# Performance work log

Measured on AMD Instinct MI355X. Metric: run time of the kernel, lower is better.

## Reference

```python
import jax, jax.numpy as jnp
import numpy as np

# Model dims: D=input_dim, H=hidden_dim, E=num_experts, k=1
B, T, D, H, E = 4, 1024, 1024, 4096, 8
ALPHA = BETA = GAMMA = 0.001


def setup_inputs() -> dict:
    key = jax.random.key(0)
    ks = jax.random.split(key, 6)
    s = 0.02
    return {
        "x": jax.random.normal(ks[0], (B, T, D), jnp.float32),
        "gate_w": jax.random.normal(ks[1], (D, E), jnp.float32) * s,
        "gate_b": jnp.zeros((E,), jnp.float32),
        "w1": jax.random.normal(ks[2], (E, D, H), jnp.float32) * s,
        "b1": jnp.zeros((E, H), jnp.float32),
        "w2": jax.random.normal(ks[3], (E, H, D), jnp.float32) * s,
        "b2": jnp.zeros((E, D), jnp.float32),
    }


def reference(x, gate_w, gate_b, w1, b1, w2, b2):
    Bs, Ts, Ds = x.shape
    N = Bs * Ts
    nE = gate_w.shape[1]
    xf = x.reshape(N, Ds)

    logits = xf @ gate_w + gate_b                      # (N, E)
    probs = jax.nn.softmax(logits, axis=-1)            # (N, E)
    # k=1 top-k == argmax
    top1 = jnp.argmax(logits, axis=-1)                 # (N,) int
    top1_p = jnp.take_along_axis(probs, top1[:, None], axis=-1)[:, 0]  # (N,)
    m = jax.nn.one_hot(top1, nE, dtype=x.dtype)        # (N, E) routing mask
    counts = m.sum(axis=0)                             # (E,) tokens per expert
    safe = jnp.maximum(counts, 1.0)

    # Dense per-expert FFN on all tokens (baseline for sparse dispatch)
    h = jax.nn.relu(jnp.einsum('nd,edh->enh', xf, w1) + b1[:, None, :])   # (E,N,H)
    y = jnp.einsum('enh,ehd->end', h, w2) + b2[:, None, :]                # (E,N,D)

    # Per-expert scalar avg prob of selected tokens (module multiplies by the MEAN prob)
    avg_p = jnp.where(counts > 0, (m * top1_p[:, None]).sum(axis=0) / safe, 0.0)  # (E,)
    out = jnp.einsum('ne,e,end->nd', m, avg_p, y)      # masked combine

    # Load-balancing aux loss
    usage = counts / N
    aux_loss = (usage ** 2).sum() * nE

    # Orthogonality loss: for each expert, G = Y_e Y_e^T over its tokens,
    # mean of squared off-diagonals. Computed via ||Y^T Y||_F^2 trick (DxD)
    ym = y * jnp.transpose(m)[:, :, None]              # (E,N,D) masked outputs
    M = jnp.einsum('end,enc->edc', ym, ym)             # (E,D,D) = Y^T Y per expert
    sq_norms = (ym ** 2).sum(axis=-1)                  # (E,N) diag of Gram
    off_sq_sum = (M ** 2).sum(axis=(1, 2)) - (sq_norms ** 2).sum(axis=1)  # (E,)
    orth_loss = jnp.where(counts > 0, off_sq_sum / (safe ** 2), 0.0).sum()

    # Variance loss
    var_loss = -((probs - probs.mean(axis=0)) ** 2).mean()

    total_loss = ALPHA * aux_loss + BETA * orth_loss + GAMMA * var_loss
    return out.reshape(Bs, Ts, Ds), total_loss
```

## Files before the change

kernel.cpp:

```cpp
#include <hip/hip_runtime.h>
#include <stdint.h>

#define TOKENS 4096
#define DIM    1024
#define HDIM   4096
#define NEXP   8
#define NPAD   5120
#define ALPHA  0.001f
#define BETA   0.001f
#define GAMMA  0.001f

#define WS_CNT      0
#define WS_SUMP     32
#define WS_PSUM     64
#define WS_PSUMSQ   96
#define WS_OFFP     128
#define WS_AVGP     192
#define WS_LOSSP    224
#define WS_OFFSQ    256
#define WS_HDR_END  512
#define WS_YNORM    512
#define WS_LIST     21504
#define WS_XB       152576
#define WS_W1T      8541184
#define WS_W2T      75650048
#define WS_HBUF     142758912
#define WS_YT       184701952
#define WS_TOTAL    195187712

typedef __bf16 bf16x8 __attribute__((ext_vector_type(8)));
typedef float  f32x4  __attribute__((ext_vector_type(4)));
typedef unsigned short u16x4 __attribute__((ext_vector_type(4)));

__device__ __forceinline__ unsigned short f2bf(float f) {
    union { float f; unsigned u; } v; v.f = f;
    unsigned r = v.u + 0x7fffu + ((v.u >> 16) & 1u);
    return (unsigned short)(r >> 16);
}
__device__ __forceinline__ float bf2f(unsigned short h) {
    union { unsigned u; float f; } v; v.u = ((unsigned)h) << 16;
    return v.f;
}

__global__ void k_cvt_x(const float* __restrict__ x, unsigned short* __restrict__ xb) {
    const int n4 = TOKENS * DIM / 4;
    for (int i = blockIdx.x * blockDim.x + threadIdx.x; i < n4; i += gridDim.x * blockDim.x) {
        float4 v = ((const float4*)x)[i];
        u16x4 o;
        o[0] = f2bf(v.x); o[1] = f2bf(v.y); o[2] = f2bf(v.z); o[3] = f2bf(v.w);
        ((u16x4*)xb)[i] = o;
    }
}

__global__ void k_transpose_cvt(const float* __restrict__ in, unsigned short* __restrict__ out,
                                int R, int C) {
    __shared__ float tile[32][33];
    const float* inp = in + (size_t)blockIdx.z * R * C;
    unsigned short* outp = out + (size_t)blockIdx.z * R * C;
    int r0 = blockIdx.y * 32, c0 = blockIdx.x * 32;
    int tx = threadIdx.x & 31, ty = threadIdx.x >> 5;
#pragma unroll
    for (int j = 0; j < 4; j++)
        tile[ty + 8 * j][tx] = inp[(size_t)(r0 + ty + 8 * j) * C + c0 + tx];
    __syncthreads();
#pragma unroll
    for (int j = 0; j < 4; j++)
        outp[(size_t)(c0 + ty + 8 * j) * R + r0 + tx] = f2bf(tile[tx][ty + 8 * j]);
}

__global__ __launch_bounds__(1024) void k_gate(
        const float* __restrict__ x, const float* __restrict__ gw, const float* __restrict__ gb,
        int* __restrict__ cnt, float* __restrict__ sump,
        float* __restrict__ psum, float* __restrict__ psumsq, int* __restrict__ list) {
    __shared__ float gwT[NEXP * DIM];
    __shared__ float bacc[3 * NEXP];
    int tid = threadIdx.x;
    if (tid < 3 * NEXP) bacc[tid] = 0.f;
    for (int i = tid; i < DIM * NEXP; i += 1024) {
        int d = i >> 3, e = i & 7;
        gwT[e * DIM + d] = gw[i];
    }
    __syncthreads();
    int wv = tid >> 6, l = tid & 63;
    int t = blockIdx.x * 16 + wv;
    float acc[8];
#pragma unroll
    for (int e = 0; e < 8; e++) acc[e] = 0.f;
    const float* xr = x + (size_t)t * DIM;
#pragma unroll
    for (int j = 0; j < 16; j++) {
        float xv = xr[l + 64 * j];
#pragma unroll
        for (int e = 0; e < 8; e++) acc[e] += xv * gwT[e * DIM + l + 64 * j];
    }
#pragma unroll
    for (int e = 0; e < 8; e++) {
#pragma unroll
        for (int s = 32; s > 0; s >>= 1) acc[e] += __shfl_xor(acc[e], s);
    }
    if (l == 0) {
        float lg[8], mx = -1e30f;
#pragma unroll
        for (int e = 0; e < 8; e++) { lg[e] = acc[e] + gb[e]; mx = fmaxf(mx, lg[e]); }
        float p[8], se = 0.f;
#pragma unroll
        for (int e = 0; e < 8; e++) { p[e] = __expf(lg[e] - mx); se += p[e]; }
        float inv = 1.f / se;
        int arg = 0; float best = lg[0];
#pragma unroll
        for (int e = 1; e < 8; e++) if (lg[e] > best) { best = lg[e]; arg = e; }
        float ptop = p[arg] * inv;
        int pos = atomicAdd(&cnt[arg], 1);
        list[arg * TOKENS + pos] = t;
        atomicAdd(&bacc[arg], ptop);
#pragma unroll
        for (int e = 0; e < 8; e++) {
            float pe = p[e] * inv;
            atomicAdd(&bacc[8 + e], pe);
            atomicAdd(&bacc[16 + e], pe * pe);
        }
    }
    __syncthreads();
    if (tid < 8) {
        atomicAdd(&sump[tid], bacc[tid]);
        atomicAdd(&psum[tid], bacc[8 + tid]);
        atomicAdd(&psumsq[tid], bacc[16 + tid]);
    }
}

__global__ void k_finalize_gate(const int* __restrict__ cnt, const float* __restrict__ sump,
                                const float* __restrict__ psum, const float* __restrict__ psumsq,
                                int* __restrict__ offp, float* __restrict__ avgp,
                                float* __restrict__ lossp) {
    if (threadIdx.x == 0) {
        int off = 0; float aux = 0.f, var = 0.f;
        for (int e = 0; e < 8; e++) {
            offp[e] = off;
            int c = cnt[e];
            off += ((c + 127) / 128) * 128;
            float cf = (float)c;
            avgp[e] = (c > 0) ? sump[e] / cf : 0.f;
            float u = cf / (float)TOKENS;
            aux += u * u;
            var += psumsq[e] - psum[e] * psum[e] / (float)TOKENS;
        }
        offp[8] = off;
        aux *= (float)NEXP;
        float varloss = -var / ((float)TOKENS * (float)NEXP);
        lossp[0] = ALPHA * aux + GAMMA * varloss;
    }
}

__global__ __launch_bounds__(256) void k_gemm1(
        const unsigned short* __restrict__ xb, const unsigned short* __restrict__ w1t,
        const float* __restrict__ b1, const int* __restrict__ cnt, const int* __restrict__ offp,
        const int* __restrict__ list, unsigned short* __restrict__ Hbuf) {
    int e = blockIdx.z, rt = blockIdx.y, ct = blockIdx.x;
    int cnt_e = cnt[e];
    int row0 = rt * 128;
    if (row0 >= cnt_e) return;
    int offe = offp[e];
    __shared__ unsigned short ldsA[128 * 32];
    __shared__ unsigned short ldsB[128 * 32];
    int tid = threadIdx.x, wv = tid >> 6, l = tid & 63;
    int wr = wv >> 1, wc = wv & 1;
    int r0s = l, r1s = 64 + l;
    int t0 = list[e * TOKENS + min(row0 + r0s, cnt_e - 1)];
    int t1 = list[e * TOKENS + min(row0 + r1s, cnt_e - 1)];
    const unsigned short* srcA0 = xb + (size_t)t0 * DIM + wv * 8;
    const unsigned short* srcA1 = xb + (size_t)t1 * DIM + wv * 8;
    const unsigned short* srcB0 = w1t + ((size_t)e * HDIM + ct * 128 + r0s) * DIM + wv * 8;
    const unsigned short* srcB1 = w1t + ((size_t)e * HDIM + ct * 128 + r1s) * DIM + wv * 8;
    f32x4 acc[4][4] = {};
    for (int kk = 0; kk < DIM; kk += 32) {
        bf16x8 va0 = *(const bf16x8*)(srcA0 + kk);
        bf16x8 va1 = *(const bf16x8*)(srcA1 + kk);
        bf16x8 vb0 = *(const bf16x8*)(srcB0 + kk);
        bf16x8 vb1 = *(const bf16x8*)(srcB1 + kk);
        __syncthreads();
        *(bf16x8*)(ldsA + (wv * 128 + l) * 8)      = va0;
        *(bf16x8*)(ldsA + (wv * 128 + 64 + l) * 8) = va1;
        *(bf16x8*)(ldsB + (wv * 128 + l) * 8)      = vb0;
        *(bf16x8*)(ldsB + (wv * 128 + 64 + l) * 8) = vb1;
        __syncthreads();
        int g = l >> 4, rr = l & 15;
        bf16x8 a[4], b[4];
#pragma unroll
        for (int m = 0; m < 4; m++) a[m] = *(const bf16x8*)(ldsA + (g * 128 + wr * 64 + m * 16 + rr) * 8);
#pragma unroll
        for (int n = 0; n < 4; n++) b[n] = *(const bf16x8*)(ldsB + (g * 128 + wc * 64 + n * 16 + rr) * 8);
#pragma unroll
        for (int m = 0; m < 4; m++)
#pragma unroll
            for (int n = 0; n < 4; n++)
                acc[m][n] = __builtin_amdgcn_mfma_f32_16x16x32_bf16(a[m], b[n], acc[m][n], 0, 0, 0);
    }
    int g = l >> 4, rr = l & 15;
#pragma unroll
    for (int n = 0; n < 4; n++) {
        int colg = ct * 128 + wc * 64 + n * 16 + rr;
        float bv = b1[e * HDIM + colg];
#pragma unroll
        for (int m = 0; m < 4; m++) {
#pragma unroll
            for (int j = 0; j < 4; j++) {
                int rloc = row0 + wr * 64 + m * 16 + g * 4 + j;
                if (rloc < cnt_e) {
                    float v = fmaxf(acc[m][n][j] + bv, 0.f);
                    Hbuf[(size_t)(offe + rloc) * HDIM + colg] = f2bf(v);
                }
            }
        }
    }
}

__global__ __launch_bounds__(256) void k_gemm2(
        const unsigned short* __restrict__ Hbuf, const unsigned short* __restrict__ w2t,
        const float* __restrict__ b2, const int* __restrict__ cnt, const int* __restrict__ offp,
        const int* __restrict__ list, const float* __restrict__ avgp,
        float* __restrict__ out, unsigned short* __restrict__ yT) {
    int e = blockIdx.z, rt = blockIdx.y, ct = blockIdx.x;
    int cnt_e = cnt[e];
    int row0 = rt * 128;
    if (row0 >= cnt_e) return;
    int offe = offp[e];
    __shared__ unsigned short ldsA[128 * 32];
    __shared__ unsigned short ldsB[128 * 32];
    int tid = threadIdx.x, wv = tid >> 6, l = tid & 63;
    int wr = wv >> 1, wc = wv & 1;
    int r0s = l, r1s = 64 + l;
    const unsigned short* srcA0 = Hbuf + (size_t)(offe + row0 + r0s) * HDIM + wv * 8;
    const unsigned short* srcA1 = Hbuf + (size_t)(offe + row0 + r1s) * HDIM + wv * 8;
    const unsigned short* srcB0 = w2t + ((size_t)e * DIM + ct * 128 + r0s) * HDIM + wv * 8;
    const unsigned short* srcB1 = w2t + ((size_t)e * DIM + ct * 128 + r1s) * HDIM + wv * 8;
    f32x4 acc[4][4] = {};
    for (int kk = 0; kk < HDIM; kk += 32) {
        bf16x8 va0 = *(const bf16x8*)(srcA0 + kk);
        bf16x8 va1 = *(const bf16x8*)(srcA1 + kk);
        bf16x8 vb0 = *(const bf16x8*)(srcB0 + kk);
        bf16x8 vb1 = *(const bf16x8*)(srcB1 + kk);
        __syncthreads();
        *(bf16x8*)(ldsA + (wv * 128 + l) * 8)      = va0;
        *(bf16x8*)(ldsA + (wv * 128 + 64 + l) * 8) = va1;
        *(bf16x8*)(ldsB + (wv * 128 + l) * 8)      = vb0;
        *(bf16x8*)(ldsB + (wv * 128 + 64 + l) * 8) = vb1;
        __syncthreads();
        int g = l >> 4, rr = l & 15;
        bf16x8 a[4], b[4];
#pragma unroll
        for (int m = 0; m < 4; m++) a[m] = *(const bf16x8*)(ldsA + (g * 128 + wr * 64 + m * 16 + rr) * 8);
#pragma unroll
        for (int n = 0; n < 4; n++) b[n] = *(const bf16x8*)(ldsB + (g * 128 + wc * 64 + n * 16 + rr) * 8);
#pragma unroll
        for (int m = 0; m < 4; m++)
#pragma unroll
            for (int n = 0; n < 4; n++)
                acc[m][n] = __builtin_amdgcn_mfma_f32_16x16x32_bf16(a[m], b[n], acc[m][n], 0, 0, 0);
    }
    float ap = avgp[e];
    int g = l >> 4, rr = l & 15;
#pragma unroll
    for (int m = 0; m < 4; m++) {
        int rbase = row0 + wr * 64 + m * 16 + g * 4;
        int toks[4]; bool lv[4];
#pragma unroll
        for (int j = 0; j < 4; j++) {
            int rl = rbase + j;
            lv[j] = rl < cnt_e;
            toks[j] = lv[j] ? list[e * TOKENS + rl] : 0;
        }
#pragma unroll
        for (int n = 0; n < 4; n++) {
            int colg = ct * 128 + wc * 64 + n * 16 + rr;
            float bv = b2[e * DIM + colg];
            u16x4 pk;
#pragma unroll
            for (int j = 0; j < 4; j++) {
                float yv = acc[m][n][j] + bv;
                if (lv[j]) {
                    out[(size_t)toks[j] * DIM + colg] = ap * yv;
                    pk[j] = f2bf(yv);
                } else {
                    pk[j] = 0;
                }
            }
            *(u16x4*)(yT + (size_t)colg * NPAD + offe + rbase) = pk;
        }
    }
}

__global__ void k_ynorm(const unsigned short* __restrict__ yT, float* __restrict__ ynorm) {
    int n = blockIdx.x * blockDim.x + threadIdx.x;
    if (n >= NPAD) return;
    float s = 0.f;
    for (int d = 0; d < DIM; d++) {
        float v = bf2f(yT[(size_t)d * NPAD + n]);
        s += v * v;
    }
    ynorm[n] = s;
}

__global__ __launch_bounds__(256) void k_gram(
        const unsigned short* __restrict__ yT, const int* __restrict__ cnt,
        const int* __restrict__ offp, float* __restrict__ offsq) {
    int e = blockIdx.z, dt = blockIdx.y, ct = blockIdx.x;
    int cnt_e = cnt[e];
    if (cnt_e <= 0) return;
    int offe = offp[e];
    int ksteps = (cnt_e + 31) / 32;
    __shared__ unsigned short ldsA[128 * 32];
    __shared__ unsigned short ldsB[128 * 32];
    __shared__ float wsum[4];
    int tid = threadIdx.x, wv = tid >> 6, l = tid & 63;
    int wr = wv >> 1, wc = wv & 1;
    int r0s = l, r1s = 64 + l;
    const unsigned short* srcA0 = yT + (size_t)(dt * 128 + r0s) * NPAD + offe + wv * 8;
    const unsigned short* srcA1 = yT + (size_t)(dt * 128 + r1s) * NPAD + offe + wv * 8;
    const unsigned short* srcB0 = yT + (size_t)(ct * 128 + r0s) * NPAD + offe + wv * 8;
    const unsigned short* srcB1 = yT + (size_t)(ct * 128 + r1s) * NPAD + offe + wv * 8;
    f32x4 acc[4][4] = {};
    for (int ks = 0; ks < ksteps; ks++) {
        int kk = ks * 32;
        bf16x8 va0 = *(const bf16x8*)(srcA0 + kk);
        bf16x8 va1 = *(const bf16x8*)(srcA1 + kk);
        bf16x8 vb0 = *(const bf16x8*)(srcB0 + kk);
        bf16x8 vb1 = *(const bf16x8*)(srcB1 + kk);
        __syncthreads();
        *(bf16x8*)(ldsA + (wv * 128 + l) * 8)      = va0;
        *(bf16x8*)(ldsA + (wv * 128 + 64 + l) * 8) = va1;
        *(bf16x8*)(ldsB + (wv * 128 + l) * 8)      = vb0;
        *(bf16x8*)(ldsB + (wv * 128 + 64 + l) * 8) = vb1;
        __syncthreads();
        int g = l >> 4, rr = l & 15;
        bf16x8 a[4], b[4];
#pragma unroll
        for (int m = 0; m < 4; m++) a[m] = *(const bf16x8*)(ldsA + (g * 128 + wr * 64 + m * 16 + rr) * 8);
#pragma unroll
        for (int n = 0; n < 4; n++) b[n] = *(const bf16x8*)(ldsB + (g * 128 + wc * 64 + n * 16 + rr) * 8);
#pragma unroll
        for (int m = 0; m < 4; m++)
#pragma unroll
            for (int n = 0; n < 4; n++)
                acc[m][n] = __builtin_amdgcn_mfma_f32_16x16x32_bf16(a[m], b[n], acc[m][n], 0, 0, 0);
    }
    float s = 0.f;
#pragma unroll
    for (int m = 0; m < 4; m++)
#pragma unroll
        for (int n = 0; n < 4; n++)
#pragma unroll
            for (int j = 0; j < 4; j++) s += acc[m][n][j] * acc[m][n][j];
#pragma unroll
    for (int sh = 32; sh > 0; sh >>= 1) s += __shfl_xor(s, sh);
    if (l == 0) wsum[wv] = s;
    __syncthreads();
    if (tid == 0) atomicAdd(&offsq[e], wsum[0] + wsum[1] + wsum[2] + wsum[3]);
}

__global__ void k_loss(const int* __restrict__ cnt, const int* __restrict__ offp,
                       const float* __restrict__ offsq, const float* __restrict__ ynorm,
                       const float* __restrict__ lossp, float* __restrict__ out_loss) {
    __shared__ float ssq[8];
    int tid = threadIdx.x;
    if (tid < 8) ssq[tid] = 0.f;
    __syncthreads();
    int total = offp[8];
    for (int i = tid; i < total; i += blockDim.x) {
        int e = 0;
#pragma unroll
        for (int k = 0; k < 8; k++) if (i >= offp[k + 1]) e = k + 1;
        float s = ynorm[i];
        atomicAdd(&ssq[e], s * s);
    }
    __syncthreads();
    if (tid == 0) {
        float orth = 0.f;
        for (int e = 0; e < 8; e++) {
            if (cnt[e] > 0) {
                float cf = (float)cnt[e];
                orth += (offsq[e] - ssq[e]) / (cf * cf);
            }
        }
        out_loss[0] = lossp[0] + BETA * orth;
    }
}

extern "C" void kernel_launch(void* const* d_in, const int* in_sizes, int n_in,
                              void* d_out, int out_size, void* d_ws, size_t ws_size,
                              hipStream_t stream) {
    (void)in_sizes; (void)n_in; (void)out_size;
    const float* x  = (const float*)d_in[0];
    const float* gw = (const float*)d_in[1];
    const float* gb = (const float*)d_in[2];
    const float* w1 = (const float*)d_in[3];
    const float* b1 = (const float*)d_in[4];
    const float* w2 = (const float*)d_in[5];
    const float* b2 = (const float*)d_in[6];
    float* out = (float*)d_out;
    char* ws = (char*)d_ws;
    if (ws_size < (size_t)WS_TOTAL) return;

    int*   cnt    = (int*)(ws + WS_CNT);
    float* sump   = (float*)(ws + WS_SUMP);
    float* psum   = (float*)(ws + WS_PSUM);
    float* psumsq = (float*)(ws + WS_PSUMSQ);
    int*   offp   = (int*)(ws + WS_OFFP);
    float* avgp   = (float*)(ws + WS_AVGP);
    float* lossp  = (float*)(ws + WS_LOSSP);
    float* offsq  = (float*)(ws + WS_OFFSQ);
    float* ynorm  = (float*)(ws + WS_YNORM);
    int*   list   = (int*)(ws + WS_LIST);
    unsigned short* xb   = (unsigned short*)(ws + WS_XB);
    unsigned short* w1t  = (unsigned short*)(ws + WS_W1T);
    unsigned short* w2t  = (unsigned short*)(ws + WS_W2T);
    unsigned short* Hbuf = (unsigned short*)(ws + WS_HBUF);
    unsigned short* yT   = (unsigned short*)(ws + WS_YT);

    hipMemsetAsync(ws, 0, WS_HDR_END, stream);
    k_cvt_x<<<2048, 256, 0, stream>>>(x, xb);
    k_transpose_cvt<<<dim3(128, 32, 8), 256, 0, stream>>>(w1, w1t, 1024, 4096);
    k_transpose_cvt<<<dim3(32, 128, 8), 256, 0, stream>>>(w2, w2t, 4096, 1024);
    k_gate<<<256, 1024, 0, stream>>>(x, gw, gb, cnt, sump, psum, psumsq, list);
    k_finalize_gate<<<1, 64, 0, stream>>>(cnt, sump, psum, psumsq, offp, avgp, lossp);
    k_gemm1<<<dim3(32, 32, 8), 256, 0, stream>>>(xb, w1t, b1, cnt, offp, list, Hbuf);
    k_gemm2<<<dim3(8, 32, 8), 256, 0, stream>>>(Hbuf, w2t, b2, cnt, offp, list, avgp, out, yT);
    k_ynorm<<<20, 256, 0, stream>>>(yT, ynorm);
    k_gram<<<dim3(8, 8, 8), 256, 0, stream>>>(yT, cnt, offp, offsq);
    k_loss<<<1, 256, 0, stream>>>(cnt, offp, offsq, ynorm, lossp, out + (size_t)TOKENS * DIM);
}
```

Baseline: 858.9 us.

## Compact grids, register double-buffer GEMMs, split-K gemm2, fuse combine and ynorm

The GEMM grids are compacted so each block derives its expert from the padded row offset instead of launching empty blocks per expert. All three MFMA kernels gain a two-stage register prefetch of global loads. gemm2 is split in two along K, writing fp32 partials into a buffer that reuses the w1t region. A new combine kernel sums the partials, adds the bias, scatters the scaled output and writes yT, and accumulates row norms with atomics, which replaces the separate ynorm kernel. The transpose now uses 64x64 tiles. The cost is extra fp32 partial-buffer traffic, atomics, and reuse of the w1t region, which is safe only because gemm1 has finished by then.

```diff
diff --git a/kernel.cpp b/kernel.cpp
--- a/kernel.cpp
+++ b/kernel.cpp
@@ -18,8 +18,8 @@
 #define WS_AVGP     192
 #define WS_LOSSP    224
 #define WS_OFFSQ    256
-#define WS_HDR_END  512
 #define WS_YNORM    512
+#define WS_ZERO_END 20992
 #define WS_LIST     21504
 #define WS_XB       152576
 #define WS_W1T      8541184
@@ -27,6 +27,8 @@
 #define WS_HBUF     142758912
 #define WS_YT       184701952
 #define WS_TOTAL    195187712
+#define WS_YBUF     WS_W1T
+#define YBS         (NPAD * DIM)
 
 typedef __bf16 bf16x8 __attribute__((ext_vector_type(8)));
 typedef float  f32x4  __attribute__((ext_vector_type(4)));
@@ -36,10 +38,6 @@
     union { float f; unsigned u; } v; v.f = f;
     unsigned r = v.u + 0x7fffu + ((v.u >> 16) & 1u);
     return (unsigned short)(r >> 16);
-}
-__device__ __forceinline__ float bf2f(unsigned short h) {
-    union { unsigned u; float f; } v; v.u = ((unsigned)h) << 16;
-    return v.f;
 }
 
 __global__ void k_cvt_x(const float* __restrict__ x, unsigned short* __restrict__ xb) {
@@ -52,20 +50,20 @@
     }
 }
 
-__global__ void k_transpose_cvt(const float* __restrict__ in, unsigned short* __restrict__ out,
-                                int R, int C) {
-    __shared__ float tile[32][33];
+__global__ __launch_bounds__(256) void k_transpose_cvt(
+        const float* __restrict__ in, unsigned short* __restrict__ out, int R, int C) {
+    __shared__ float tile[64][65];
     const float* inp = in + (size_t)blockIdx.z * R * C;
     unsigned short* outp = out + (size_t)blockIdx.z * R * C;
-    int r0 = blockIdx.y * 32, c0 = blockIdx.x * 32;
-    int tx = threadIdx.x & 31, ty = threadIdx.x >> 5;
-#pragma unroll
-    for (int j = 0; j < 4; j++)
-        tile[ty + 8 * j][tx] = inp[(size_t)(r0 + ty + 8 * j) * C + c0 + tx];
-    __syncthreads();
-#pragma unroll
-    for (int j = 0; j < 4; j++)
-        outp[(size_t)(c0 + ty + 8 * j) * R + r0 + tx] = f2bf(tile[tx][ty + 8 * j]);
+    int r0 = blockIdx.y * 64, c0 = blockIdx.x * 64;
+    int tx = threadIdx.x & 63, ty = threadIdx.x >> 6;
+#pragma unroll
+    for (int j = 0; j < 16; j++)
+        tile[ty + 4 * j][tx] = inp[(size_t)(r0 + ty + 4 * j) * C + c0 + tx];
+    __syncthreads();
+#pragma unroll
+    for (int j = 0; j < 16; j++)
+        outp[(size_t)(c0 + ty + 4 * j) * R + r0 + tx] = f2bf(tile[tx][ty + 4 * j]);
 }
 
 __global__ __launch_bounds__(1024) void k_gate(
@@ -155,34 +153,49 @@
         const unsigned short* __restrict__ xb, const unsigned short* __restrict__ w1t,
         const float* __restrict__ b1, const int* __restrict__ cnt, const int* __restrict__ offp,
         const int* __restrict__ list, unsigned short* __restrict__ Hbuf) {
-    int e = blockIdx.z, rt = blockIdx.y, ct = blockIdx.x;
-    int cnt_e = cnt[e];
-    int row0 = rt * 128;
-    if (row0 >= cnt_e) return;
-    int offe = offp[e];
     __shared__ unsigned short ldsA[128 * 32];
     __shared__ unsigned short ldsB[128 * 32];
+    int ct = blockIdx.x, rt = blockIdx.y;
+    int prow0 = rt * 128;
+    if (prow0 >= offp[8]) return;
+    int e = 0;
+#pragma unroll
+    for (int k = 1; k < 8; k++) if (prow0 >= offp[k]) e = k;
+    int offe = offp[e], row0 = prow0 - offe, cnt_e = cnt[e];
     int tid = threadIdx.x, wv = tid >> 6, l = tid & 63;
     int wr = wv >> 1, wc = wv & 1;
-    int r0s = l, r1s = 64 + l;
-    int t0 = list[e * TOKENS + min(row0 + r0s, cnt_e - 1)];
-    int t1 = list[e * TOKENS + min(row0 + r1s, cnt_e - 1)];
+    int t0 = list[e * TOKENS + min(row0 + l, cnt_e - 1)];
+    int t1 = list[e * TOKENS + min(row0 + 64 + l, cnt_e - 1)];
     const unsigned short* srcA0 = xb + (size_t)t0 * DIM + wv * 8;
     const unsigned short* srcA1 = xb + (size_t)t1 * DIM + wv * 8;
-    const unsigned short* srcB0 = w1t + ((size_t)e * HDIM + ct * 128 + r0s) * DIM + wv * 8;
-    const unsigned short* srcB1 = w1t + ((size_t)e * HDIM + ct * 128 + r1s) * DIM + wv * 8;
+    const unsigned short* srcB0 = w1t + ((size_t)e * HDIM + ct * 128 + l) * DIM + wv * 8;
+    const unsigned short* srcB1 = w1t + ((size_t)e * HDIM + ct * 128 + 64 + l) * DIM + wv * 8;
     f32x4 acc[4][4] = {};
-    for (int kk = 0; kk < DIM; kk += 32) {
-        bf16x8 va0 = *(const bf16x8*)(srcA0 + kk);
-        bf16x8 va1 = *(const bf16x8*)(srcA1 + kk);
-        bf16x8 vb0 = *(const bf16x8*)(srcB0 + kk);
-        bf16x8 vb1 = *(const bf16x8*)(srcB1 + kk);
-        __syncthreads();
-        *(bf16x8*)(ldsA + (wv * 128 + l) * 8)      = va0;
-        *(bf16x8*)(ldsA + (wv * 128 + 64 + l) * 8) = va1;
-        *(bf16x8*)(ldsB + (wv * 128 + l) * 8)      = vb0;
-        *(bf16x8*)(ldsB + (wv * 128 + 64 + l) * 8) = vb1;
-        __syncthreads();
+    bf16x8 sa0[2], sa1[2], sb0[2], sb1[2];
+    const int NK = DIM / 32;
+#pragma unroll
+    for (int p = 0; p < 2; p++) {
+        int kk = p * 32;
+        sa0[p] = *(const bf16x8*)(srcA0 + kk);
+        sa1[p] = *(const bf16x8*)(srcA1 + kk);
+        sb0[p] = *(const bf16x8*)(srcB0 + kk);
+        sb1[p] = *(const bf16x8*)(srcB1 + kk);
+    }
+    for (int i = 0; i < NK; i++) {
+        int cur = i & 1;
+        __syncthreads();
+        *(bf16x8*)(ldsA + (wv * 128 + l) * 8)      = sa0[cur];
+        *(bf16x8*)(ldsA + (wv * 128 + 64 + l) * 8) = sa1[cur];
+        *(bf16x8*)(ldsB + (wv * 128 + l) * 8)      = sb0[cur];
+        *(bf16x8*)(ldsB + (wv * 128 + 64 + l) * 8) = sb1[cur];
+        __syncthreads();
+        if (i + 2 < NK) {
+            int kk = (i + 2) * 32;
+            sa0[cur] = *(const bf16x8*)(srcA0 + kk);
+            sa1[cur] = *(const bf16x8*)(srcA1 + kk);
+            sb0[cur] = *(const bf16x8*)(srcB0 + kk);
+            sb1[cur] = *(const bf16x8*)(srcB1 + kk);
+        }
         int g = l >> 4, rr = l & 15;
         bf16x8 a[4], b[4];
 #pragma unroll
@@ -216,35 +229,50 @@
 
 __global__ __launch_bounds__(256) void k_gemm2(
         const unsigned short* __restrict__ Hbuf, const unsigned short* __restrict__ w2t,
-        const float* __restrict__ b2, const int* __restrict__ cnt, const int* __restrict__ offp,
-        const int* __restrict__ list, const float* __restrict__ avgp,
-        float* __restrict__ out, unsigned short* __restrict__ yT) {
-    int e = blockIdx.z, rt = blockIdx.y, ct = blockIdx.x;
-    int cnt_e = cnt[e];
-    int row0 = rt * 128;
-    if (row0 >= cnt_e) return;
-    int offe = offp[e];
+        const int* __restrict__ cnt, const int* __restrict__ offp,
+        float* __restrict__ ybuf) {
     __shared__ unsigned short ldsA[128 * 32];
     __shared__ unsigned short ldsB[128 * 32];
+    int ct = blockIdx.x, rt = blockIdx.y, s = blockIdx.z;
+    int prow0 = rt * 128;
+    if (prow0 >= offp[8]) return;
+    int e = 0;
+#pragma unroll
+    for (int k = 1; k < 8; k++) if (prow0 >= offp[k]) e = k;
+    int offe = offp[e];
     int tid = threadIdx.x, wv = tid >> 6, l = tid & 63;
     int wr = wv >> 1, wc = wv & 1;
-    int r0s = l, r1s = 64 + l;
-    const unsigned short* srcA0 = Hbuf + (size_t)(offe + row0 + r0s) * HDIM + wv * 8;
-    const unsigned short* srcA1 = Hbuf + (size_t)(offe + row0 + r1s) * HDIM + wv * 8;
-    const unsigned short* srcB0 = w2t + ((size_t)e * DIM + ct * 128 + r0s) * HDIM + wv * 8;
-    const unsigned short* srcB1 = w2t + ((size_t)e * DIM + ct * 128 + r1s) * HDIM + wv * 8;
+    const size_t kbase = (size_t)s * (HDIM / 2) + wv * 8;
+    const unsigned short* srcA0 = Hbuf + (size_t)(prow0 + l) * HDIM + kbase;
+    const unsigned short* srcA1 = Hbuf + (size_t)(prow0 + 64 + l) * HDIM + kbase;
+    const unsigned short* srcB0 = w2t + ((size_t)e * DIM + ct * 128 + l) * HDIM + kbase;
+    const unsigned short* srcB1 = w2t + ((size_t)e * DIM + ct * 128 + 64 + l) * HDIM + kbase;
     f32x4 acc[4][4] = {};
-    for (int kk = 0; kk < HDIM; kk += 32) {
-        bf16x8 va0 = *(const bf16x8*)(srcA0 + kk);
-        bf16x8 va1 = *(const bf16x8*)(srcA1 + kk);
-        bf16x8 vb0 = *(const bf16x8*)(srcB0 + kk);
-        bf16x8 vb1 = *(const bf16x8*)(srcB1 + kk);
-        __syncthreads();
-        *(bf16x8*)(ldsA + (wv * 128 + l) * 8)      = va0;
-        *(bf16x8*)(ldsA + (wv * 128 + 64 + l) * 8) = va1;
-        *(bf16x8*)(ldsB + (wv * 128 + l) * 8)      = vb0;
-        *(bf16x8*)(ldsB + (wv * 128 + 64 + l) * 8) = vb1;
-        __syncthreads();
+    bf16x8 sa0[2], sa1[2], sb0[2], sb1[2];
+    const int NK = HDIM / 2 / 32;
+#pragma unroll
+    for (int p = 0; p < 2; p++) {
+        int kk = p * 32;
+        sa0[p] = *(const bf16x8*)(srcA0 + kk);
+        sa1[p] = *(const bf16x8*)(srcA1 + kk);
+        sb0[p] = *(const bf16x8*)(srcB0 + kk);
+        sb1[p] = *(const bf16x8*)(srcB1 + kk);
+    }
+    for (int i = 0; i < NK; i++) {
+        int cur = i & 1;
+        __syncthreads();
+        *(bf16x8*)(ldsA + (wv * 128 + l) * 8)      = sa0[cur];
+        *(bf16x8*)(ldsA + (wv * 128 + 64 + l) * 8) = sa1[cur];
+        *(bf16x8*)(ldsB + (wv * 128 + l) * 8)      = sb0[cur];
+        *(bf16x8*)(ldsB + (wv * 128 + 64 + l) * 8) = sb1[cur];
+        __syncthreads();
+        if (i + 2 < NK) {
+            int kk = (i + 2) * 32;
+            sa0[cur] = *(const bf16x8*)(srcA0 + kk);
+            sa1[cur] = *(const bf16x8*)(srcA1 + kk);
+            sb0[cur] = *(const bf16x8*)(srcB0 + kk);
+            sb1[cur] = *(const bf16x8*)(srcB1 + kk);
+        }
         int g = l >> 4, rr = l & 15;
         bf16x8 a[4], b[4];
 #pragma unroll
@@ -257,80 +285,105 @@
             for (int n = 0; n < 4; n++)
                 acc[m][n] = __builtin_amdgcn_mfma_f32_16x16x32_bf16(a[m], b[n], acc[m][n], 0, 0, 0);
     }
-    float ap = avgp[e];
+    float* yb = ybuf + (size_t)s * YBS;
     int g = l >> 4, rr = l & 15;
 #pragma unroll
-    for (int m = 0; m < 4; m++) {
-        int rbase = row0 + wr * 64 + m * 16 + g * 4;
-        int toks[4]; bool lv[4];
-#pragma unroll
-        for (int j = 0; j < 4; j++) {
-            int rl = rbase + j;
-            lv[j] = rl < cnt_e;
-            toks[j] = lv[j] ? list[e * TOKENS + rl] : 0;
-        }
+    for (int m = 0; m < 4; m++)
 #pragma unroll
         for (int n = 0; n < 4; n++) {
             int colg = ct * 128 + wc * 64 + n * 16 + rr;
-            float bv = b2[e * DIM + colg];
-            u16x4 pk;
 #pragma unroll
             for (int j = 0; j < 4; j++) {
-                float yv = acc[m][n][j] + bv;
-                if (lv[j]) {
-                    out[(size_t)toks[j] * DIM + colg] = ap * yv;
-                    pk[j] = f2bf(yv);
-                } else {
-                    pk[j] = 0;
-                }
+                int prow = prow0 + wr * 64 + m * 16 + g * 4 + j;
+                yb[(size_t)prow * DIM + colg] = acc[m][n][j];
             }
-            *(u16x4*)(yT + (size_t)colg * NPAD + offe + rbase) = pk;
-        }
-    }
-}
-
-__global__ void k_ynorm(const unsigned short* __restrict__ yT, float* __restrict__ ynorm) {
-    int n = blockIdx.x * blockDim.x + threadIdx.x;
-    if (n >= NPAD) return;
-    float s = 0.f;
-    for (int d = 0; d < DIM; d++) {
-        float v = bf2f(yT[(size_t)d * NPAD + n]);
-        s += v * v;
-    }
-    ynorm[n] = s;
+        }
+}
+
+__global__ __launch_bounds__(256) void k_combine(
+        const float* __restrict__ ybuf, const float* __restrict__ b2,
+        const int* __restrict__ cnt, const int* __restrict__ offp,
+        const int* __restrict__ list, const float* __restrict__ avgp,
+        float* __restrict__ out, unsigned short* __restrict__ yT,
+        float* __restrict__ ynorm) {
+    int dt = blockIdx.x, rt = blockIdx.y;
+    int prow0 = rt * 128;
+    if (prow0 >= offp[8]) return;
+    int e = 0;
+#pragma unroll
+    for (int k = 1; k < 8; k++) if (prow0 >= offp[k]) e = k;
+    int offe = offp[e], cnt_e = cnt[e];
+    float ap = avgp[e];
+    int tid = threadIdx.x, l = tid & 63, w = tid >> 6;
+    int d = dt * 64 + l;
+    float bv = b2[e * DIM + d];
+    for (int q = w * 8; q < w * 8 + 8; q++) {
+        int prow = prow0 + q * 4;
+        u16x4 pk;
+        float ys2[4];
+#pragma unroll
+        for (int j = 0; j < 4; j++) {
+            int pr = prow + j;
+            int rl = pr - offe;
+            float yv = ybuf[(size_t)pr * DIM + d] + ybuf[(size_t)YBS + (size_t)pr * DIM + d] + bv;
+            bool valid = rl < cnt_e;
+            if (valid) out[(size_t)list[e * TOKENS + rl] * DIM + d] = ap * yv;
+            pk[j] = valid ? f2bf(yv) : (unsigned short)0;
+            ys2[j] = valid ? yv * yv : 0.f;
+        }
+        *(u16x4*)(yT + (size_t)d * NPAD + prow) = pk;
+#pragma unroll
+        for (int j = 0; j < 4; j++) {
+            float sv = ys2[j];
+#pragma unroll
+            for (int sh = 32; sh > 0; sh >>= 1) sv += __shfl_xor(sv, sh);
+            if (l == 0) atomicAdd(&ynorm[prow + j], sv);
+        }
+    }
 }
 
 __global__ __launch_bounds__(256) void k_gram(
         const unsigned short* __restrict__ yT, const int* __restrict__ cnt,
         const int* __restrict__ offp, float* __restrict__ offsq) {
+    __shared__ unsigned short ldsA[128 * 32];
+    __shared__ unsigned short ldsB[128 * 32];
+    __shared__ float wsum[4];
     int e = blockIdx.z, dt = blockIdx.y, ct = blockIdx.x;
     int cnt_e = cnt[e];
     if (cnt_e <= 0) return;
     int offe = offp[e];
-    int ksteps = (cnt_e + 31) / 32;
-    __shared__ unsigned short ldsA[128 * 32];
-    __shared__ unsigned short ldsB[128 * 32];
-    __shared__ float wsum[4];
+    int NK = (offp[e + 1] - offe) >> 5;
     int tid = threadIdx.x, wv = tid >> 6, l = tid & 63;
     int wr = wv >> 1, wc = wv & 1;
-    int r0s = l, r1s = 64 + l;
-    const unsigned short* srcA0 = yT + (size_t)(dt * 128 + r0s) * NPAD + offe + wv * 8;
-    const unsigned short* srcA1 = yT + (size_t)(dt * 128 + r1s) * NPAD + offe + wv * 8;
-    const unsigned short* srcB0 = yT + (size_t)(ct * 128 + r0s) * NPAD + offe + wv * 8;
-    const unsigned short* srcB1 = yT + (size_t)(ct * 128 + r1s) * NPAD + offe + wv * 8;
+    const unsigned short* srcA0 = yT + (size_t)(dt * 128 + l) * NPAD + offe + wv * 8;
+    const unsigned short* srcA1 = yT + (size_t)(dt * 128 + 64 + l) * NPAD + offe + wv * 8;
+    const unsigned short* srcB0 = yT + (size_t)(ct * 128 + l) * NPAD + offe + wv * 8;
+    const unsigned short* srcB1 = yT + (size_t)(ct * 128 + 64 + l) * NPAD + offe + wv * 8;
     f32x4 acc[4][4] = {};
-    for (int ks = 0; ks < ksteps; ks++) {
-        int kk = ks * 32;
-        bf16x8 va0 = *(const bf16x8*)(srcA0 + kk);
-        bf16x8 va1 = *(const bf16x8*)(srcA1 + kk);
-        bf16x8 vb0 = *(const bf16x8*)(srcB0 + kk);
-        bf16x8 vb1 = *(const bf16x8*)(srcB1 + kk);
-        __syncthreads();
-        *(bf16x8*)(ldsA + (wv * 128 + l) * 8)      = va0;
-        *(bf16x8*)(ldsA + (wv * 128 + 64 + l) * 8) = va1;
-        *(bf16x8*)(ldsB + (wv * 128 + l) * 8)      = vb0;
-        *(bf16x8*)(ldsB + (wv * 128 + 64 + l) * 8) = vb1;
-        __syncthreads();
+    bf16x8 sa0[2], sa1[2], sb0[2], sb1[2];
+#pragma unroll
+    for (int p = 0; p < 2; p++) {
+        int kk = p * 32;
+        sa0[p] = *(const bf16x8*)(srcA0 + kk);
+        sa1[p] = *(const bf16x8*)(srcA1 + kk);
+        sb0[p] = *(const bf16x8*)(srcB0 + kk);
+        sb1[p] = *(const bf16x8*)(srcB1 + kk);
+    }
+    for (int i = 0; i < NK; i++) {
+        int cur = i & 1;
+        __syncthreads();
+        *(bf16x8*)(ldsA + (wv * 128 + l) * 8)      = sa0[cur];
+        *(bf16x8*)(ldsA + (wv * 128 + 64 + l) * 8) = sa1[cur];
+        *(bf16x8*)(ldsB + (wv * 128 + l) * 8)      = sb0[cur];
+        *(bf16x8*)(ldsB + (wv * 128 + 64 + l) * 8) = sb1[cur];
+        __syncthreads();
+        if (i + 2 < NK) {
+            int kk = (i + 2) * 32;
+            sa0[cur] = *(const bf16x8*)(srcA0 + kk);
+            sa1[cur] = *(const bf16x8*)(srcA1 + kk);
+            sb0[cur] = *(const bf16x8*)(srcB0 + kk);
+            sb1[cur] = *(const bf16x8*)(srcB1 + kk);
+        }
         int g = l >> 4, rr = l & 15;
         bf16x8 a[4], b[4];
 #pragma unroll
@@ -415,16 +468,17 @@
     unsigned short* w2t  = (unsigned short*)(ws + WS_W2T);
     unsigned short* Hbuf = (unsigned short*)(ws + WS_HBUF);
     unsigned short* yT   = (unsigned short*)(ws + WS_YT);
-
-    hipMemsetAsync(ws, 0, WS_HDR_END, stream);
+    float* ybuf          = (float*)(ws + WS_YBUF);
+
+    hipMemsetAsync(ws, 0, WS_ZERO_END, stream);
     k_cvt_x<<<2048, 256, 0, stream>>>(x, xb);
-    k_transpose_cvt<<<dim3(128, 32, 8), 256, 0, stream>>>(w1, w1t, 1024, 4096);
-    k_transpose_cvt<<<dim3(32, 128, 8), 256, 0, stream>>>(w2, w2t, 4096, 1024);
+    k_transpose_cvt<<<dim3(64, 16, 8), 256, 0, stream>>>(w1, w1t, 1024, 4096);
+    k_transpose_cvt<<<dim3(16, 64, 8), 256, 0, stream>>>(w2, w2t, 4096, 1024);
     k_gate<<<256, 1024, 0, stream>>>(x, gw, gb, cnt, sump, psum, psumsq, list);
     k_finalize_gate<<<1, 64, 0, stream>>>(cnt, sump, psum, psumsq, offp, avgp, lossp);
-    k_gemm1<<<dim3(32, 32, 8), 256, 0, stream>>>(xb, w1t, b1, cnt, offp, list, Hbuf);
-    k_gemm2<<<dim3(8, 32, 8), 256, 0, stream>>>(Hbuf, w2t, b2, cnt, offp, list, avgp, out, yT);
-    k_ynorm<<<20, 256, 0, stream>>>(yT, ynorm);
+    k_gemm1<<<dim3(32, 40), 256, 0, stream>>>(xb, w1t, b1, cnt, offp, list, Hbuf);
+    k_gemm2<<<dim3(8, 40, 2), 256, 0, stream>>>(Hbuf, w2t, cnt, offp, ybuf);
+    k_combine<<<dim3(16, 40), 256, 0, stream>>>(ybuf, b2, cnt, offp, list, avgp, out, yT, ynorm);
     k_gram<<<dim3(8, 8, 8), 256, 0, stream>>>(yT, cnt, offp, offsq);
     k_loss<<<1, 256, 0, stream>>>(cnt, offp, offsq, ynorm, lossp, out + (size_t)TOKENS * DIM);
 }
```

Measured after the change: 1.456 ms. +69.6%, slower.
